# Optimization experiments

Hardware: AMD Instinct MI355X
Metric: run time of the kernel (lower is better)

The kernel has to match this reference:

```python
import jax, jax.numpy as jnp
import numpy as np

N_NODES = 50000
HEADS = 4
OUT_DIM = 64
NEG_SLOPE = 0.2
BETA = 0.5
C_CONST = 1.0
EPS = 1e-16


def setup_inputs() -> dict:
    key = jax.random.key(0)
    ks = jax.random.split(key, 6)
    in_dim = 128
    x = jax.random.normal(ks[0], (N_NODES, in_dim), dtype=jnp.float32)
    edge_index = jax.random.randint(ks[1], (2, 800000), 0, N_NODES, dtype=jnp.int64)
    # GATConv params (glorot-ish scale)
    W = jax.random.normal(ks[2], (in_dim, HEADS * OUT_DIM), dtype=jnp.float32) * (1.0 / np.sqrt(in_dim))
    att_src = jax.random.normal(ks[3], (HEADS, OUT_DIM), dtype=jnp.float32) * (1.0 / np.sqrt(OUT_DIM))
    att_dst = jax.random.normal(ks[4], (HEADS, OUT_DIM), dtype=jnp.float32) * (1.0 / np.sqrt(OUT_DIM))
    bias = jnp.zeros((HEADS * OUT_DIM,), dtype=jnp.float32)
    return {"x": x, "edge_index": edge_index, "W": W, "att_src": att_src,
            "att_dst": att_dst, "bias": bias}


def _gat_conv(x, edge_index, W, att_src, att_dst, bias):
    N = x.shape[0]
    # add self loops (PyG GATConv default)
    loop = jnp.arange(N, dtype=edge_index.dtype)
    src = jnp.concatenate([edge_index[0], loop])
    dst = jnp.concatenate([edge_index[1], loop])
    # linear transform: [N, H, F]
    h = (x @ W).reshape(N, HEADS, OUT_DIM)
    # per-node attention logits: [N, H]
    a_src = jnp.einsum('nhf,hf->nh', h, att_src)
    a_dst = jnp.einsum('nhf,hf->nh', h, att_dst)
    # per-edge logits and segment softmax over destination nodes
    e = jax.nn.leaky_relu(a_src[src] + a_dst[dst], negative_slope=NEG_SLOPE)  # [E, H]
    m = jax.ops.segment_max(e, dst, num_segments=N)                           # [N, H]
    ex = jnp.exp(e - m[dst])
    s = jax.ops.segment_sum(ex, dst, num_segments=N)                          # [N, H]
    alpha = ex / (s[dst] + EPS)                                               # [E, H]
    # aggregate messages: [N, H, F]
    out = jax.ops.segment_sum(alpha[:, :, None] * h[src], dst, num_segments=N)
    return out.reshape(N, HEADS * OUT_DIM) + bias


def reference(x, edge_index, W, att_src, att_dst, bias):
    # eval mode: feature dropout and attention dropout are identity
    z = _gat_conv(x, edge_index, W, att_src, att_dst, bias)
    return BETA * z + (C_CONST - BETA) * jax.nn.elu(z)
```

## Files before the change

### kernel.cpp

```cpp
#include <hip/hip_runtime.h>
#include <hip/hip_bf16.h>

typedef unsigned short u16;
typedef __attribute__((ext_vector_type(8))) short bf16x8;
typedef __attribute__((ext_vector_type(4))) float f32x4;

#define HEADS 4
#define OUT_DIM 64
#define HF 256
#define IN_DIM 128
#define NEG_SLOPE 0.2f
#define EPSF 1e-16f

__device__ __forceinline__ float braw2f(u16 u) {
    union { float f; unsigned int i; } c; c.i = ((unsigned int)u) << 16; return c.f;
}
__device__ __forceinline__ u16 f2braw(float v) {
    __hip_bfloat16 t = __float2bfloat16(v);
    return *(u16*)&t;
}
__device__ __forceinline__ float lrelu(float e) { return e < 0.f ? NEG_SLOPE * e : e; }

__device__ __forceinline__ bool detect_i64(const int* ei) {
    return (ei[1] | ei[3] | ei[5] | ei[7] | ei[9] | ei[11] | ei[13] | ei[15]) == 0;
}
__device__ __forceinline__ void get_edge(const int* ei, int E, int t, bool i64,
                                         int& s, int& d) {
    if (t < E) {
        if (i64) { s = ei[2 * t]; d = ei[2 * (E + t)]; }
        else     { s = ei[t];     d = ei[E + t]; }
    } else {
        s = d = t - E;
    }
}

__global__ __launch_bounds__(256) void init_kernel(const float* __restrict__ W,
                                                   const float* __restrict__ att_s,
                                                   const float* __restrict__ att_d,
                                                   float* __restrict__ wa_s,
                                                   float* __restrict__ wa_d,
                                                   int* __restrict__ cnt,
                                                   int* __restrict__ cur,
                                                   int* __restrict__ gcnt,
                                                   int* __restrict__ hist,
                                                   int* __restrict__ bcur,
                                                   int N, int NZ) {
    int b = blockIdx.x;
    if (b == 0) {
        if (threadIdx.x == 0) *gcnt = 0;
        hist[threadIdx.x] = 0;
        bcur[threadIdx.x] = 0;
    }
    if (b < NZ) {
        int i = b * 256 + threadIdx.x;
        if (i < N) { cnt[i] = 0; cur[i] = 0; }
    } else {
        for (int idx = threadIdx.x; idx < HEADS * IN_DIM; idx += 256) {
            int h = idx >> 7, k = idx & 127;
            float ss = 0.f, sd = 0.f;
            for (int f = 0; f < OUT_DIM; ++f) {
                float wv = W[k * HF + h * OUT_DIM + f];
                ss = fmaf(wv, att_s[h * OUT_DIM + f], ss);
                sd = fmaf(wv, att_d[h * OUT_DIM + f], sd);
            }
            wa_s[idx] = ss;
            wa_d[idx] = sd;
        }
    }
}

__global__ __launch_bounds__(256) void phase1_kernel(const float* __restrict__ x,
                                                     const int* __restrict__ ei,
                                                     const float* __restrict__ W,
                                                     const float* __restrict__ wa_s,
                                                     const float* __restrict__ wa_d,
                                                     float* __restrict__ a_src,
                                                     float* __restrict__ a_dst,
                                                     u16* __restrict__ xb,
                                                     u16* __restrict__ Wfrag,
                                                     int* __restrict__ cnt,
                                                     int N, int E, int NA, int NC) {
    int b = blockIdx.x;
    if (b < NA) {
        int wid = threadIdx.x >> 6;
        int l = threadIdx.x & 63;
        int g = l >> 4, c = l & 15, kc = c * 8;
        int v = b * 16 + wid * 4 + g;
        if (v >= N) return;

        const float4* xr = (const float4*)(x + (size_t)v * IN_DIM + kc);
        float4 x0 = xr[0], x1 = xr[1];

        uint4 u;
        u.x = (unsigned)f2braw(x0.x) | ((unsigned)f2braw(x0.y) << 16);
        u.y = (unsigned)f2braw(x0.z) | ((unsigned)f2braw(x0.w) << 16);
        u.z = (unsigned)f2braw(x1.x) | ((unsigned)f2braw(x1.y) << 16);
        u.w = (unsigned)f2braw(x1.z) | ((unsigned)f2braw(x1.w) << 16);
        *(uint4*)(xb + (size_t)v * IN_DIM + kc) = u;

        float ps[4], pd[4];
        #pragma unroll
        for (int h = 0; h < 4; ++h) {
            const float4* s4 = (const float4*)(wa_s + h * IN_DIM + kc);
            const float4* d4 = (const float4*)(wa_d + h * IN_DIM + kc);
            float4 s0 = s4[0], s1 = s4[1], d0 = d4[0], d1 = d4[1];
            ps[h] = x0.x*s0.x + x0.y*s0.y + x0.z*s0.z + x0.w*s0.w
                  + x1.x*s1.x + x1.y*s1.y + x1.z*s1.z + x1.w*s1.w;
            pd[h] = x0.x*d0.x + x0.y*d0.y + x0.z*d0.z + x0.w*d0.w
                  + x1.x*d1.x + x1.y*d1.y + x1.z*d1.z + x1.w*d1.w;
        }
        #pragma unroll
        for (int off = 1; off < 16; off <<= 1) {
            #pragma unroll
            for (int h = 0; h < 4; ++h) {
                ps[h] += __shfl_xor(ps[h], off);
                pd[h] += __shfl_xor(pd[h], off);
            }
        }
        if (c == 0) {
            float4 vs, vd;
            vs.x = ps[0]; vs.y = ps[1]; vs.z = ps[2]; vs.w = ps[3];
            vd.x = pd[0]; vd.y = pd[1]; vd.z = pd[2]; vd.w = pd[3];
            *(float4*)(a_src + (size_t)v * HEADS) = vs;
            *(float4*)(a_dst + (size_t)v * HEADS) = vd;
        }
    } else if (b < NA + NC) {
        int t = (b - NA) * 256 + threadIdx.x;
        if (t >= E + N) return;
        bool i64 = detect_i64(ei);
        int src, dst; get_edge(ei, E, t, i64, src, dst);
        if (src >= 0 && src < N && dst >= 0 && dst < N) atomicAdd(cnt + dst, 1);
    } else {
        int bb = b - NA - NC;
        for (int idx = bb * 256 + threadIdx.x; idx < 32768; idx += 8 * 256) {
            int j = idx & 7, l = (idx >> 3) & 63, t = (idx >> 9) & 3;
            int s = (idx >> 11) & 3, h = (idx >> 13) & 3;
            int k = s * 32 + ((l >> 4) & 3) * 8 + j;
            int col = h * OUT_DIM + t * 16 + (l & 15);
            Wfrag[idx] = f2braw(W[k * HF + col]);
        }
    }
}

__global__ __launch_bounds__(256) void offset_kernel(const int* __restrict__ cnt,
                                                     int* __restrict__ offs,
                                                     int* __restrict__ gcnt,
                                                     int* __restrict__ hist, int N) {
    __shared__ int lh[256];
    lh[threadIdx.x] = 0;
    __syncthreads();

    int idx = blockIdx.x * 256 + threadIdx.x;
    int l = threadIdx.x & 63;
    int d = (idx < N) ? cnt[idx] : 0;
    if (idx < N) atomicAdd(lh + min(max(d, 0), 255), 1);

    int s = d;
    #pragma unroll
    for (int off = 1; off < 64; off <<= 1) {
        int t = __shfl_up(s, off);
        if (l >= off) s += t;
    }
    int base = 0;
    if (l == 63) base = atomicAdd(gcnt, s);
    base = __shfl(base, 63);
    if (idx < N) offs[idx] = base + s - d;

    __syncthreads();
    if (lh[threadIdx.x]) atomicAdd(hist + threadIdx.x, lh[threadIdx.x]);
}

__global__ __launch_bounds__(256) void fillscatter_kernel(const int* __restrict__ ei,
                                                          const int* __restrict__ offs,
                                                          int* __restrict__ cur,
                                                          int* __restrict__ slots,
                                                          uint2* __restrict__ wslots,
                                                          const float* __restrict__ a_src,
                                                          const float* __restrict__ a_dst,
                                                          const int* __restrict__ cnt,
                                                          const int* __restrict__ hist,
                                                          int* __restrict__ bcur,
                                                          int* __restrict__ perm,
                                                          int E, int N, int NC) {
    __shared__ int sc[256];
    __shared__ int lh[256];
    __shared__ int lbase[256];

    int b = blockIdx.x;
    if (b < NC) {
        int t = b * 256 + threadIdx.x;
        if (t >= E + N) return;
        bool i64 = detect_i64(ei);
        int src, dst; get_edge(ei, E, t, i64, src, dst);
        if (src >= 0 && src < N && dst >= 0 && dst < N) {
            int pos = atomicAdd(cur + dst, 1);
            int idx = offs[dst] + pos;
            slots[idx] = src;
            if (wslots) {
                float4 as = ((const float4*)a_src)[src];
                float4 ad = ((const float4*)a_dst)[dst];
                float w0 = __expf(lrelu(as.x + ad.x));
                float w1 = __expf(lrelu(as.y + ad.y));
                float w2 = __expf(lrelu(as.z + ad.z));
                float w3 = __expf(lrelu(as.w + ad.w));
                uint2 wp;
                wp.x = (unsigned)f2braw(w0) | ((unsigned)f2braw(w1) << 16);
                wp.y = (unsigned)f2braw(w2) | ((unsigned)f2braw(w3) << 16);
                wslots[idx] = wp;
            }
        }
    } else {
        int tid = threadIdx.x;
        sc[tid] = hist[tid];
        lh[tid] = 0;
        __syncthreads();
        #pragma unroll
        for (int off = 1; off < 256; off <<= 1) {
            int tv = (tid >= off) ? sc[tid - off] : 0;
            __syncthreads();
            sc[tid] += tv;
            __syncthreads();
        }

        int idx = (b - NC) * 256 + tid;
        int bk = 0, mypos = 0;
        bool valid = (idx < N);
        if (valid) {
            bk = min(max(cnt[idx], 0), 255);
            mypos = atomicAdd(lh + bk, 1);
        }
        __syncthreads();
        int c = lh[tid];
        if (c) lbase[tid] = atomicAdd(bcur + tid, c);
        __syncthreads();
        if (valid) {
            int p = (N - sc[bk]) + lbase[bk] + mypos;
            if (p >= 0 && p < N) perm[p] = idx;
        }
    }
}

#define ACC_EDGE(wp, r) do { \
    float w0_ = braw2f((wp).x & 0xffff), w1_ = braw2f((wp).x >> 16); \
    float w2_ = braw2f((wp).y & 0xffff), w3_ = braw2f((wp).y >> 16); \
    ls0 += w0_; ls1 += w1_; ls2 += w2_; ls3 += w3_; \
    float xv_[8]; \
    xv_[0] = braw2f((r).x & 0xffff); xv_[1] = braw2f((r).x >> 16); \
    xv_[2] = braw2f((r).y & 0xffff); xv_[3] = braw2f((r).y >> 16); \
    xv_[4] = braw2f((r).z & 0xffff); xv_[5] = braw2f((r).z >> 16); \
    xv_[6] = braw2f((r).w & 0xffff); xv_[7] = braw2f((r).w >> 16); \
    _Pragma("unroll") \
    for (int q_ = 0; q_ < 8; ++q_) { \
        G0[q_] = fmaf(w0_, xv_[q_], G0[q_]); \
        G1[q_] = fmaf(w1_, xv_[q_], G1[q_]); \
        G2[q_] = fmaf(w2_, xv_[q_], G2[q_]); \
        G3[q_] = fmaf(w3_, xv_[q_], G3[q_]); \
    } \
} while (0)

__global__ __launch_bounds__(512) void fused_gz_kernel(const int* __restrict__ perm,
                                                       const int* __restrict__ offs,
                                                       const int* __restrict__ cnt,
                                                       const int* __restrict__ slots,
                                                       const uint2* __restrict__ wslots,
                                                       const u16* __restrict__ xb,
                                                       const u16* __restrict__ Wfrag,
                                                       const float* __restrict__ bias,
                                                       float* __restrict__ out,
                                                       int N, int ET) {
    __shared__ u16 smem[32 * 520];
    __shared__ int pvals[32];

    int tid = threadIdx.x;
    int wid = tid >> 6;
    int l = tid & 63;
    int g = l >> 4, c = l & 15, kc = c * 8;
    int n = wid * 4 + g;
    int pidx = blockIdx.x * 32 + n;

    int v = -1;
    if (pidx < N) {
        v = perm[pidx];
        if (v < 0 || v >= N) v = -1;
    }
    if (c == 0) pvals[n] = v;

    int beg = 0, end = 0;
    if (v >= 0) {
        beg = offs[v];
        int deg = cnt[v];
        beg = max(0, min(beg, ET));
        end = max(beg, min(beg + deg, ET));
    }

    float ls0 = 0.f, ls1 = 0.f, ls2 = 0.f, ls3 = 0.f;
    float G0[8] = {0,0,0,0,0,0,0,0};
    float G1[8] = {0,0,0,0,0,0,0,0};
    float G2[8] = {0,0,0,0,0,0,0,0};
    float G3[8] = {0,0,0,0,0,0,0,0};

    int j = beg;
    int sn0 = 0, sn1 = 0, sn2 = 0, sn3 = 0;
    uint2 wn0 = {0,0}, wn1 = {0,0}, wn2 = {0,0}, wn3 = {0,0};
    if (j + 4 <= end) {
        sn0 = slots[j];     sn1 = slots[j + 1];
        sn2 = slots[j + 2]; sn3 = slots[j + 3];
        wn0 = wslots[j];     wn1 = wslots[j + 1];
        wn2 = wslots[j + 2]; wn3 = wslots[j + 3];
    }
    for (; j + 8 <= end; j += 4) {
        int s0 = sn0, s1 = sn1, s2 = sn2, s3 = sn3;
        uint2 wp0 = wn0, wp1 = wn1, wp2 = wn2, wp3 = wn3;
        uint4 r0 = *(const uint4*)(xb + (size_t)s0 * IN_DIM + kc);
        uint4 r1 = *(const uint4*)(xb + (size_t)s1 * IN_DIM + kc);
        uint4 r2 = *(const uint4*)(xb + (size_t)s2 * IN_DIM + kc);
        uint4 r3 = *(const uint4*)(xb + (size_t)s3 * IN_DIM + kc);
        sn0 = slots[j + 4]; sn1 = slots[j + 5];
        sn2 = slots[j + 6]; sn3 = slots[j + 7];
        wn0 = wslots[j + 4]; wn1 = wslots[j + 5];
        wn2 = wslots[j + 6]; wn3 = wslots[j + 7];
        ACC_EDGE(wp0, r0);
        ACC_EDGE(wp1, r1);
        ACC_EDGE(wp2, r2);
        ACC_EDGE(wp3, r3);
    }
    if (j + 4 <= end) {
        uint4 r0 = *(const uint4*)(xb + (size_t)sn0 * IN_DIM + kc);
        uint4 r1 = *(const uint4*)(xb + (size_t)sn1 * IN_DIM + kc);
        uint4 r2 = *(const uint4*)(xb + (size_t)sn2 * IN_DIM + kc);
        uint4 r3 = *(const uint4*)(xb + (size_t)sn3 * IN_DIM + kc);
        ACC_EDGE(wn0, r0);
        ACC_EDGE(wn1, r1);
        ACC_EDGE(wn2, r2);
        ACC_EDGE(wn3, r3);
        j += 4;
    }
    for (; j < end; ++j) {
        int s0 = slots[j];
        uint2 wp0 = wslots[j];
        uint4 r0 = *(const uint4*)(xb + (size_t)s0 * IN_DIM + kc);
        ACC_EDGE(wp0, r0);
    }

    if (v >= 0) {
        float i0 = 1.f / (ls0 + EPSF), i1 = 1.f / (ls1 + EPSF);
        float i2 = 1.f / (ls2 + EPSF), i3 = 1.f / (ls3 + EPSF);
        u16* lp = smem + n * 520 + c * 8;
        #pragma unroll
        for (int h = 0; h < 4; ++h) {
            const float* G = h == 0 ? G0 : h == 1 ? G1 : h == 2 ? G2 : G3;
            float inv = h == 0 ? i0 : h == 1 ? i1 : h == 2 ? i2 : i3;
            uint4 u;
            u.x = (unsigned)f2braw(G[0] * inv) | ((unsigned)f2braw(G[1] * inv) << 16);
            u.y = (unsigned)f2braw(G[2] * inv) | ((unsigned)f2braw(G[3] * inv) << 16);
            u.z = (unsigned)f2braw(G[4] * inv) | ((unsigned)f2braw(G[5] * inv) << 16);
            u.w = (unsigned)f2braw(G[6] * inv) | ((unsigned)f2braw(G[7] * inv) << 16);
            *(uint4*)(lp + h * 128) = u;
        }
    }
    __syncthreads();

    int t = wid >> 2;
    int h = wid & 3;
    int q = l >> 4, mcol = l & 15;

    const u16* lp = smem + (t * 16 + mcol) * 520 + h * 128 + q * 8;
    bf16x8 A[4];
    A[0] = *(const bf16x8*)(lp);
    A[1] = *(const bf16x8*)(lp + 32);
    A[2] = *(const bf16x8*)(lp + 64);
    A[3] = *(const bf16x8*)(lp + 96);

    f32x4 acc0 = {0.f,0.f,0.f,0.f}, acc1 = acc0, acc2 = acc0, acc3 = acc0;
    #pragma unroll
    for (int s = 0; s < 4; ++s) {
        const u16* wb = Wfrag + (((h * 4 + s) * 4) << 9) + l * 8;
        bf16x8 B0 = *(const bf16x8*)(wb);
        bf16x8 B1 = *(const bf16x8*)(wb + 512);
        bf16x8 B2 = *(const bf16x8*)(wb + 1024);
        bf16x8 B3 = *(const bf16x8*)(wb + 1536);
        acc0 = __builtin_amdgcn_mfma_f32_16x16x32_bf16(A[s], B0, acc0, 0, 0, 0);
        acc1 = __builtin_amdgcn_mfma_f32_16x16x32_bf16(A[s], B1, acc1, 0, 0, 0);
        acc2 = __builtin_amdgcn_mfma_f32_16x16x32_bf16(A[s], B2, acc2, 0, 0, 0);
        acc3 = __builtin_amdgcn_mfma_f32_16x16x32_bf16(A[s], B3, acc3, 0, 0, 0);
    }

    #pragma unroll
    for (int bt = 0; bt < 4; ++bt) {
        f32x4 a = bt == 0 ? acc0 : bt == 1 ? acc1 : bt == 2 ? acc2 : acc3;
        float b = bias[h * OUT_DIM + bt * 16 + mcol];
        #pragma unroll
        for (int r = 0; r < 4; ++r) {
            int vv = pvals[t * 16 + q * 4 + r];
            if (vv >= 0) {
                float z = a[r] + b;
                float y = z > 0.f ? z : 0.5f * z + 0.5f * (__expf(z) - 1.f);
                out[(size_t)vv * HF + h * OUT_DIM + bt * 16 + mcol] = y;
            }
        }
    }
}

__global__ __launch_bounds__(512) void gather_bf_kernel(const int* __restrict__ offs,
                                                        const int* __restrict__ cnt,
                                                        const int* __restrict__ slots,
                                                        const u16* __restrict__ xb,
                                                        const float* __restrict__ a_src,
                                                        const float* __restrict__ a_dst,
                                                        u16* __restrict__ Gout, int N, int ET) {
    int v = (blockIdx.x * 512 + threadIdx.x) >> 6;
    int l = threadIdx.x & 63;
    if (v >= N) return;
    int h = l >> 4, c = l & 15, kc = c * 8;

    int beg = offs[v];
    int deg = cnt[v];
    beg = max(0, min(beg, ET));
    int end = max(beg, min(beg + deg, ET));
    float adh = a_dst[v * HEADS + h];

    float ls = 0.f;
    float G[8] = {0.f,0.f,0.f,0.f,0.f,0.f,0.f,0.f};

    int j = beg;
    for (; j + 4 <= end; j += 4) {
        int s0 = max(0, min(slots[j],     N - 1));
        int s1 = max(0, min(slots[j + 1], N - 1));
        int s2 = max(0, min(slots[j + 2], N - 1));
        int s3 = max(0, min(slots[j + 3], N - 1));
        float w0 = __expf(lrelu(a_src[s0 * HEADS + h] + adh));
        float w1 = __expf(lrelu(a_src[s1 * HEADS + h] + adh));
        float w2 = __expf(lrelu(a_src[s2 * HEADS + h] + adh));
        float w3 = __expf(lrelu(a_src[s3 * HEADS + h] + adh));
        uint4 r0 = *(const uint4*)(xb + (size_t)s0 * IN_DIM + kc);
        uint4 r1 = *(const uint4*)(xb + (size_t)s1 * IN_DIM + kc);
        uint4 r2 = *(const uint4*)(xb + (size_t)s2 * IN_DIM + kc);
        uint4 r3 = *(const uint4*)(xb + (size_t)s3 * IN_DIM + kc);
        ls += (w0 + w1) + (w2 + w3);
        unsigned ua[4];
        ua[0]=r0.x; ua[1]=r0.y; ua[2]=r0.z; ua[3]=r0.w;
        #pragma unroll
        for (int q = 0; q < 4; ++q) {
            G[2*q]   = fmaf(w0, braw2f(ua[q] & 0xffff), G[2*q]);
            G[2*q+1] = fmaf(w0, braw2f(ua[q] >> 16),    G[2*q+1]);
        }
        ua[0]=r1.x; ua[1]=r1.y; ua[2]=r1.z; ua[3]=r1.w;
        #pragma unroll
        for (int q = 0; q < 4; ++q) {
            G[2*q]   = fmaf(w1, braw2f(ua[q] & 0xffff), G[2*q]);
            G[2*q+1] = fmaf(w1, braw2f(ua[q] >> 16),    G[2*q+1]);
        }
        ua[0]=r2.x; ua[1]=r2.y; ua[2]=r2.z; ua[3]=r2.w;
        #pragma unroll
        for (int q = 0; q < 4; ++q) {
            G[2*q]   = fmaf(w2, braw2f(ua[q] & 0xffff), G[2*q]);
            G[2*q+1] = fmaf(w2, braw2f(ua[q] >> 16),    G[2*q+1]);
        }
        ua[0]=r3.x; ua[1]=r3.y; ua[2]=r3.z; ua[3]=r3.w;
        #pragma unroll
        for (int q = 0; q < 4; ++q) {
            G[2*q]   = fmaf(w3, braw2f(ua[q] & 0xffff), G[2*q]);
            G[2*q+1] = fmaf(w3, braw2f(ua[q] >> 16),    G[2*q+1]);
        }
    }
    for (; j < end; ++j) {
        int s0 = max(0, min(slots[j], N - 1));
        float w0 = __expf(lrelu(a_src[s0 * HEADS + h] + adh));
        uint4 r0 = *(const uint4*)(xb + (size_t)s0 * IN_DIM + kc);
        ls += w0;
        unsigned ua[4]; ua[0]=r0.x; ua[1]=r0.y; ua[2]=r0.z; ua[3]=r0.w;
        #pragma unroll
        for (int q = 0; q < 4; ++q) {
            G[2*q]   = fmaf(w0, braw2f(ua[q] & 0xffff), G[2*q]);
            G[2*q+1] = fmaf(w0, braw2f(ua[q] >> 16),    G[2*q+1]);
        }
    }

    float inv = 1.f / (ls + EPSF);
    uint4 u;
    u.x = (unsigned)f2braw(G[0] * inv) | ((unsigned)f2braw(G[1] * inv) << 16);
    u.y = (unsigned)f2braw(G[2] * inv) | ((unsigned)f2braw(G[3] * inv) << 16);
    u.z = (unsigned)f2braw(G[4] * inv) | ((unsigned)f2braw(G[5] * inv) << 16);
    u.w = (unsigned)f2braw(G[6] * inv) | ((unsigned)f2braw(G[7] * inv) << 16);
    *(uint4*)(Gout + (size_t)v * 512 + h * 128 + kc) = u;
}

__global__ __launch_bounds__(512) void gather_f32_kernel(const int* __restrict__ offs,
                                                         const int* __restrict__ cnt,
                                                         const int* __restrict__ slots,
                                                         const float* __restrict__ x,
                                                         const float* __restrict__ a_src,
                                                         const float* __restrict__ a_dst,
                                                         u16* __restrict__ Gout, int N, int ET) {
    int v = (blockIdx.x * 512 + threadIdx.x) >> 6;
    int l = threadIdx.x & 63;
    if (v >= N) return;
    int h = l >> 4, c = l & 15, kc = c * 8;

    int beg = offs[v];
    int deg = cnt[v];
    beg = max(0, min(beg, ET));
    int end = max(beg, min(beg + deg, ET));
    float adh = a_dst[v * HEADS + h];

    float ls = 0.f;
    float G[8] = {0.f,0.f,0.f,0.f,0.f,0.f,0.f,0.f};
    for (int j = beg; j < end; ++j) {
        int s0 = max(0, min(slots[j], N - 1));
        float w0 = __expf(lrelu(a_src[s0 * HEADS + h] + adh));
        const float4* xr0 = (const float4*)(x + (size_t)s0 * IN_DIM + kc);
        float4 a0 = xr0[0], b0 = xr0[1];
        ls += w0;
        G[0]=fmaf(w0,a0.x,G[0]); G[1]=fmaf(w0,a0.y,G[1]);
        G[2]=fmaf(w0,a0.z,G[2]); G[3]=fmaf(w0,a0.w,G[3]);
        G[4]=fmaf(w0,b0.x,G[4]); G[5]=fmaf(w0,b0.y,G[5]);
        G[6]=fmaf(w0,b0.z,G[6]); G[7]=fmaf(w0,b0.w,G[7]);
    }
    float inv = 1.f / (ls + EPSF);
    uint4 u;
    u.x = (unsigned)f2braw(G[0] * inv) | ((unsigned)f2braw(G[1] * inv) << 16);
    u.y = (unsigned)f2braw(G[2] * inv) | ((unsigned)f2braw(G[3] * inv) << 16);
    u.z = (unsigned)f2braw(G[4] * inv) | ((unsigned)f2braw(G[5] * inv) << 16);
    u.w = (unsigned)f2braw(G[6] * inv) | ((unsigned)f2braw(G[7] * inv) << 16);
    *(uint4*)(Gout + (size_t)v * 512 + h * 128 + kc) = u;
}

__global__ __launch_bounds__(256) void zgemm_kernel(const u16* __restrict__ Wfrag,
                                                    const float* __restrict__ bias,
                                                    float* __restrict__ out, int N) {
    int h = threadIdx.x >> 6;
    int l = threadIdx.x & 63;
    int q = l >> 4, mcol = l & 15;
    int nb = blockIdx.x * 16;

    const u16* G = (const u16*)out;
    bool valid = (nb + mcol) < N;
    int vA = valid ? nb + mcol : N - 1;
    const u16* gp = G + (size_t)vA * 512 + h * 128 + q * 8;
    bf16x8 A[4];
    A[0] = *(const bf16x8*)(gp);
    A[1] = *(const bf16x8*)(gp + 32);
    A[2] = *(const bf16x8*)(gp + 64);
    A[3] = *(const bf16x8*)(gp + 96);
    if (!valid) {
        bf16x8 zz = {0,0,0,0,0,0,0,0};
        A[0] = zz; A[1] = zz; A[2] = zz; A[3] = zz;
    }

    f32x4 acc0 = {0.f,0.f,0.f,0.f}, acc1 = acc0, acc2 = acc0, acc3 = acc0;
    #pragma unroll
    for (int s = 0; s < 4; ++s) {
        const u16* wb = Wfrag + (((h * 4 + s) * 4) << 9) + l * 8;
        bf16x8 B0 = *(const bf16x8*)(wb);
        bf16x8 B1 = *(const bf16x8*)(wb + 512);
        bf16x8 B2 = *(const bf16x8*)(wb + 1024);
        bf16x8 B3 = *(const bf16x8*)(wb + 1536);
        acc0 = __builtin_amdgcn_mfma_f32_16x16x32_bf16(A[s], B0, acc0, 0, 0, 0);
        acc1 = __builtin_amdgcn_mfma_f32_16x16x32_bf16(A[s], B1, acc1, 0, 0, 0);
        acc2 = __builtin_amdgcn_mfma_f32_16x16x32_bf16(A[s], B2, acc2, 0, 0, 0);
        acc3 = __builtin_amdgcn_mfma_f32_16x16x32_bf16(A[s], B3, acc3, 0, 0, 0);
    }

    #pragma unroll
    for (int t = 0; t < 4; ++t) {
        f32x4 a = t == 0 ? acc0 : t == 1 ? acc1 : t == 2 ? acc2 : acc3;
        float b = bias[h * OUT_DIM + t * 16 + mcol];
        #pragma unroll
        for (int r = 0; r < 4; ++r) {
            int v = nb + q * 4 + r;
            if (v < N) {
                float z = a[r] + b;
                float y = z > 0.f ? z : 0.5f * z + 0.5f * (__expf(z) - 1.f);
                out[(size_t)v * HF + h * OUT_DIM + t * 16 + mcol] = y;
            }
        }
    }
}

extern "C" void kernel_launch(void* const* d_in, const int* in_sizes, int n_in,
                              void* d_out, int out_size, void* d_ws, size_t ws_size,
                              hipStream_t stream) {
    const float* x       = (const float*)d_in[0];
    const int*   ei      = (const int*)d_in[1];
    const float* W       = (const float*)d_in[2];
    const float* att_src = (const float*)d_in[3];
    const float* att_dst = (const float*)d_in[4];
    const float* bias    = (const float*)d_in[5];

    const int N = in_sizes[0] / IN_DIM;
    const int E = in_sizes[1] / 2;
    const int ET = E + N;
    const int NT = (N + 255) / 256;

    char* ws = (char*)d_ws;
    size_t off = 0;
    float* wa_s   = (float*)(ws + off); off += HEADS * IN_DIM * 4;
    float* wa_d   = (float*)(ws + off); off += HEADS * IN_DIM * 4;
    u16*   Wfrag  = (u16*)(ws + off);   off += 32768 * 2;
    float* a_src  = (float*)(ws + off); off += (size_t)N * HEADS * 4;
    float* a_dst  = (float*)(ws + off); off += (size_t)N * HEADS * 4;
    int*   offs   = (int*)(ws + off);   off += ((size_t)N * 4 + 15) & ~(size_t)15;
    int*   cnt    = (int*)(ws + off);   off += ((size_t)N * 4 + 15) & ~(size_t)15;
    int*   cur    = (int*)(ws + off);   off += ((size_t)N * 4 + 15) & ~(size_t)15;
    int*   gcnt   = (int*)(ws + off);   off += 64;
    int*   hist   = (int*)(ws + off);   off += 256 * 4;
    off += 256 * 4;
    int*   bcur   = (int*)(ws + off);   off += 256 * 4;
    int*   perm   = (int*)(ws + off);   off += ((size_t)N * 4 + 15) & ~(size_t)15;
    int*   slots  = (int*)(ws + off);   off += ((size_t)ET * 4 + 15) & ~(size_t)15;
    u16*   xb     = (u16*)(ws + off);   size_t need_bf = off + (size_t)N * IN_DIM * 2;
    uint2* wslots = (uint2*)(ws + need_bf);
    size_t need_w = need_bf + (size_t)ET * 8;
    bool use_bf = (ws_size >= need_bf);
    bool use_w  = (ws_size >= need_w);

    const int NA = (N + 15) / 16;
    const int NC = (ET + 255) / 256;

    init_kernel<<<NT + 1, 256, 0, stream>>>(W, att_src, att_dst, wa_s, wa_d,
                                            cnt, cur, gcnt, hist, bcur, N, NT);
    phase1_kernel<<<NA + NC + 8, 256, 0, stream>>>(x, ei, W, wa_s, wa_d, a_src, a_dst,
                                                   use_bf ? xb : (u16*)d_out,
                                                   Wfrag, cnt, N, E, NA, NC);
    offset_kernel<<<NT, 256, 0, stream>>>(cnt, offs, gcnt, hist, N);
    fillscatter_kernel<<<NC + (use_w ? NT : 0), 256, 0, stream>>>(
        ei, offs, cur, slots, use_w ? wslots : (uint2*)0, a_src, a_dst,
        cnt, hist, bcur, perm, E, N, NC);
    if (use_w) {
        fused_gz_kernel<<<(N + 31) / 32, 512, 0, stream>>>(perm, offs, cnt, slots,
                                                           wslots, xb, Wfrag, bias,
                                                           (float*)d_out, N, ET);
    } else if (use_bf) {
        gather_bf_kernel<<<(N * 64 + 511) / 512, 512, 0, stream>>>(offs, cnt, slots, xb,
                                                                   a_src, a_dst,
                                                                   (u16*)d_out, N, ET);
        zgemm_kernel<<<(N + 15) / 16, 256, 0, stream>>>(Wfrag, bias, (float*)d_out, N);
    } else {
        gather_f32_kernel<<<(N * 64 + 511) / 512, 512, 0, stream>>>(offs, cnt, slots, x,
                                                                    a_src, a_dst,
                                                                    (u16*)d_out, N, ET);
        zgemm_kernel<<<(N + 15) / 16, 256, 0, stream>>>(Wfrag, bias, (float*)d_out, N);
    }
}
```

Before: 265.4 us.

## Split degree counters into four copies, shrink fused block, drop gather prefetch

The per-destination degree count is spread over four counter arrays picked by edge index, which cuts same-address atomic contention; offset_kernel then sums the four copies back into the first one. The fused gather+GEMM kernel moves from 32 nodes and 512 threads per block to 16 nodes and 256 threads. Its software-pipelined prefetch of slot and weight data is replaced by plain loads with clamping of source indices, and unused shared-memory rows are now zero-filled. The smaller blocks should improve occupancy and load balance, at the cost of more zero-init writes and less explicit latency hiding in the gather loop.

After: 260.1 us. 2.0% less time.

```diff
diff --git a/kernel.cpp b/kernel.cpp
--- a/kernel.cpp
+++ b/kernel.cpp
@@ -39,7 +39,7 @@
                                                    const float* __restrict__ att_d,
                                                    float* __restrict__ wa_s,
                                                    float* __restrict__ wa_d,
-                                                   int* __restrict__ cnt,
+                                                   int* __restrict__ cnt4,
                                                    int* __restrict__ cur,
                                                    int* __restrict__ gcnt,
                                                    int* __restrict__ hist,
@@ -53,7 +53,13 @@
     }
     if (b < NZ) {
         int i = b * 256 + threadIdx.x;
-        if (i < N) { cnt[i] = 0; cur[i] = 0; }
+        if (i < N) {
+            cnt4[i] = 0;
+            cnt4[N + i] = 0;
+            cnt4[2 * N + i] = 0;
+            cnt4[3 * N + i] = 0;
+            cur[i] = 0;
+        }
     } else {
         for (int idx = threadIdx.x; idx < HEADS * IN_DIM; idx += 256) {
             int h = idx >> 7, k = idx & 127;
@@ -78,7 +84,7 @@
                                                      float* __restrict__ a_dst,
                                                      u16* __restrict__ xb,
                                                      u16* __restrict__ Wfrag,
-                                                     int* __restrict__ cnt,
+                                                     int* __restrict__ cnt4,
                                                      int N, int E, int NA, int NC) {
     int b = blockIdx.x;
     if (b < NA) {
@@ -129,7 +135,8 @@
         if (t >= E + N) return;
         bool i64 = detect_i64(ei);
         int src, dst; get_edge(ei, E, t, i64, src, dst);
-        if (src >= 0 && src < N && dst >= 0 && dst < N) atomicAdd(cnt + dst, 1);
+        if (src >= 0 && src < N && dst >= 0 && dst < N)
+            atomicAdd(cnt4 + (t & 3) * N + dst, 1);
     } else {
         int bb = b - NA - NC;
         for (int idx = bb * 256 + threadIdx.x; idx < 32768; idx += 8 * 256) {
@@ -142,7 +149,7 @@
     }
 }
 
-__global__ __launch_bounds__(256) void offset_kernel(const int* __restrict__ cnt,
+__global__ __launch_bounds__(256) void offset_kernel(int* __restrict__ cnt4,
                                                      int* __restrict__ offs,
                                                      int* __restrict__ gcnt,
                                                      int* __restrict__ hist, int N) {
@@ -152,8 +159,12 @@
 
     int idx = blockIdx.x * 256 + threadIdx.x;
     int l = threadIdx.x & 63;
-    int d = (idx < N) ? cnt[idx] : 0;
-    if (idx < N) atomicAdd(lh + min(max(d, 0), 255), 1);
+    int d = 0;
+    if (idx < N) {
+        d = cnt4[idx] + cnt4[N + idx] + cnt4[2 * N + idx] + cnt4[3 * N + idx];
+        cnt4[idx] = d;
+        atomicAdd(lh + min(max(d, 0), 255), 1);
+    }
 
     int s = d;
     #pragma unroll
@@ -258,7 +269,7 @@
     } \
 } while (0)
 
-__global__ __launch_bounds__(512) void fused_gz_kernel(const int* __restrict__ perm,
+__global__ __launch_bounds__(256) void fused_gz_kernel(const int* __restrict__ perm,
                                                        const int* __restrict__ offs,
                                                        const int* __restrict__ cnt,
                                                        const int* __restrict__ slots,
@@ -268,15 +279,15 @@
                                                        const float* __restrict__ bias,
                                                        float* __restrict__ out,
                                                        int N, int ET) {
-    __shared__ u16 smem[32 * 520];
-    __shared__ int pvals[32];
+    __shared__ u16 smem[16 * 520];
+    __shared__ int pvals[16];
 
     int tid = threadIdx.x;
     int wid = tid >> 6;
     int l = tid & 63;
     int g = l >> 4, c = l & 15, kc = c * 8;
     int n = wid * 4 + g;
-    int pidx = blockIdx.x * 32 + n;
+    int pidx = blockIdx.x * 16 + n;
 
     int v = -1;
     if (pidx < N) {
@@ -300,43 +311,26 @@
     float G3[8] = {0,0,0,0,0,0,0,0};
 
     int j = beg;
-    int sn0 = 0, sn1 = 0, sn2 = 0, sn3 = 0;
-    uint2 wn0 = {0,0}, wn1 = {0,0}, wn2 = {0,0}, wn3 = {0,0};
-    if (j + 4 <= end) {
-        sn0 = slots[j];     sn1 = slots[j + 1];
-        sn2 = slots[j + 2]; sn3 = slots[j + 3];
-        wn0 = wslots[j];     wn1 = wslots[j + 1];
-        wn2 = wslots[j + 2]; wn3 = wslots[j + 3];
-    }
-    for (; j + 8 <= end; j += 4) {
-        int s0 = sn0, s1 = sn1, s2 = sn2, s3 = sn3;
-        uint2 wp0 = wn0, wp1 = wn1, wp2 = wn2, wp3 = wn3;
+    for (; j + 4 <= end; j += 4) {
+        int s0 = max(0, min(slots[j],     N - 1));
+        int s1 = max(0, min(slots[j + 1], N - 1));
+        int s2 = max(0, min(slots[j + 2], N - 1));
+        int s3 = max(0, min(slots[j + 3], N - 1));
+        uint2 wp0 = wslots[j];
+        uint2 wp1 = wslots[j + 1];
+        uint2 wp2 = wslots[j + 2];
+        uint2 wp3 = wslots[j + 3];
         uint4 r0 = *(const uint4*)(xb + (size_t)s0 * IN_DIM + kc);
         uint4 r1 = *(const uint4*)(xb + (size_t)s1 * IN_DIM + kc);
         uint4 r2 = *(const uint4*)(xb + (size_t)s2 * IN_DIM + kc);
         uint4 r3 = *(const uint4*)(xb + (size_t)s3 * IN_DIM + kc);
-        sn0 = slots[j + 4]; sn1 = slots[j + 5];
-        sn2 = slots[j + 6]; sn3 = slots[j + 7];
-        wn0 = wslots[j + 4]; wn1 = wslots[j + 5];
-        wn2 = wslots[j + 6]; wn3 = wslots[j + 7];
         ACC_EDGE(wp0, r0);
         ACC_EDGE(wp1, r1);
         ACC_EDGE(wp2, r2);
         ACC_EDGE(wp3, r3);
     }
-    if (j + 4 <= end) {
-        uint4 r0 = *(const uint4*)(xb + (size_t)sn0 * IN_DIM + kc);
-        uint4 r1 = *(const uint4*)(xb + (size_t)sn1 * IN_DIM + kc);
-        uint4 r2 = *(const uint4*)(xb + (size_t)sn2 * IN_DIM + kc);
-        uint4 r3 = *(const uint4*)(xb + (size_t)sn3 * IN_DIM + kc);
-        ACC_EDGE(wn0, r0);
-        ACC_EDGE(wn1, r1);
-        ACC_EDGE(wn2, r2);
-        ACC_EDGE(wn3, r3);
-        j += 4;
-    }
     for (; j < end; ++j) {
-        int s0 = slots[j];
+        int s0 = max(0, min(slots[j], N - 1));
         uint2 wp0 = wslots[j];
         uint4 r0 = *(const uint4*)(xb + (size_t)s0 * IN_DIM + kc);
         ACC_EDGE(wp0, r0);
@@ -357,14 +351,18 @@
             u.w = (unsigned)f2braw(G[6] * inv) | ((unsigned)f2braw(G[7] * inv) << 16);
             *(uint4*)(lp + h * 128) = u;
         }
+    } else {
+        u16* lp = smem + n * 520 + c * 8;
+        uint4 z = {0, 0, 0, 0};
+        #pragma unroll
+        for (int h = 0; h < 4; ++h) *(uint4*)(lp + h * 128) = z;
     }
     __syncthreads();
 
-    int t = wid >> 2;
-    int h = wid & 3;
+    int h = wid;
     int q = l >> 4, mcol = l & 15;
 
-    const u16* lp = smem + (t * 16 + mcol) * 520 + h * 128 + q * 8;
+    const u16* lp = smem + mcol * 520 + h * 128 + q * 8;
     bf16x8 A[4];
     A[0] = *(const bf16x8*)(lp);
     A[1] = *(const bf16x8*)(lp + 32);
@@ -391,7 +389,7 @@
         float b = bias[h * OUT_DIM + bt * 16 + mcol];
         #pragma unroll
         for (int r = 0; r < 4; ++r) {
-            int vv = pvals[t * 16 + q * 4 + r];
+            int vv = pvals[q * 4 + r];
             if (vv >= 0) {
                 float z = a[r] + b;
                 float y = z > 0.f ? z : 0.5f * z + 0.5f * (__expf(z) - 1.f);
@@ -600,11 +598,10 @@
     float* a_src  = (float*)(ws + off); off += (size_t)N * HEADS * 4;
     float* a_dst  = (float*)(ws + off); off += (size_t)N * HEADS * 4;
     int*   offs   = (int*)(ws + off);   off += ((size_t)N * 4 + 15) & ~(size_t)15;
-    int*   cnt    = (int*)(ws + off);   off += ((size_t)N * 4 + 15) & ~(size_t)15;
+    int*   cnt4   = (int*)(ws + off);   off += ((size_t)N * 16 + 15) & ~(size_t)15;
     int*   cur    = (int*)(ws + off);   off += ((size_t)N * 4 + 15) & ~(size_t)15;
     int*   gcnt   = (int*)(ws + off);   off += 64;
     int*   hist   = (int*)(ws + off);   off += 256 * 4;
-    off += 256 * 4;
     int*   bcur   = (int*)(ws + off);   off += 256 * 4;
     int*   perm   = (int*)(ws + off);   off += ((size_t)N * 4 + 15) & ~(size_t)15;
     int*   slots  = (int*)(ws + off);   off += ((size_t)ET * 4 + 15) & ~(size_t)15;
@@ -618,25 +615,25 @@
     const int NC = (ET + 255) / 256;
 
     init_kernel<<<NT + 1, 256, 0, stream>>>(W, att_src, att_dst, wa_s, wa_d,
-                                            cnt, cur, gcnt, hist, bcur, N, NT);
+                                            cnt4, cur, gcnt, hist, bcur, N, NT);
     phase1_kernel<<<NA + NC + 8, 256, 0, stream>>>(x, ei, W, wa_s, wa_d, a_src, a_dst,
                                                    use_bf ? xb : (u16*)d_out,
-                                                   Wfrag, cnt, N, E, NA, NC);
-    offset_kernel<<<NT, 256, 0, stream>>>(cnt, offs, gcnt, hist, N);
+                                                   Wfrag, cnt4, N, E, NA, NC);
+    offset_kernel<<<NT, 256, 0, stream>>>(cnt4, offs, gcnt, hist, N);
     fillscatter_kernel<<<NC + (use_w ? NT : 0), 256, 0, stream>>>(
         ei, offs, cur, slots, use_w ? wslots : (uint2*)0, a_src, a_dst,
-        cnt, hist, bcur, perm, E, N, NC);
+        cnt4, hist, bcur, perm, E, N, NC);
     if (use_w) {
-        fused_gz_kernel<<<(N + 31) / 32, 512, 0, stream>>>(perm, offs, cnt, slots,
+        fused_gz_kernel<<<(N + 15) / 16, 256, 0, stream>>>(perm, offs, cnt4, slots,
                                                            wslots, xb, Wfrag, bias,
                                                            (float*)d_out, N, ET);
     } else if (use_bf) {
-        gather_bf_kernel<<<(N * 64 + 511) / 512, 512, 0, stream>>>(offs, cnt, slots, xb,
+        gather_bf_kernel<<<(N * 64 + 511) / 512, 512, 0, stream>>>(offs, cnt4, slots, xb,
                                                                    a_src, a_dst,
                                                                    (u16*)d_out, N, ET);
         zgemm_kernel<<<(N + 15) / 16, 256, 0, stream>>>(Wfrag, bias, (float*)d_out, N);
     } else {
-        gather_f32_kernel<<<(N * 64 + 511) / 512, 512, 0, stream>>>(offs, cnt, slots, x,
+        gather_f32_kernel<<<(N * 64 + 511) / 512, 512, 0, stream>>>(offs, cnt4, slots, x,
                                                                     a_src, a_dst,
                                                                     (u16*)d_out, N, ET);
         zgemm_kernel<<<(N + 15) / 16, 256, 0, stream>>>(Wfrag, bias, (float*)d_out, N);
```
